# Optimization experiments

Hardware: AMD Instinct MI355X
Metric: run time of the kernel (lower is better)

The kernel has to match this reference:

```python
import jax, jax.numpy as jnp
import numpy as np

# Config (mirrors CorrLayerDownsample(J=3, L=8, A=1, A_prime=1, M=256, N=256,
# num_channels=1, shift_mode='samec', mask_angles=4)). With samec + 1 channel,
# every pair is 'shifted' (mask index 1) and groups (j1,j2) are contiguous in
# the global moment order, so concatenation reproduces results_storage order.
J, L, A, M, N, NB = 3, 8, 1, 256, 256, 2
MASK_ANGLES = 4
RADII = (1, 2)  # dyadic shift radii (assumed form of create_masks_shift)

def _mask_positions():
    # shift mask 1: origin plus shifts along mask_angles directions at dyadic radii
    pos = {(0, 0)}
    for k in range(MASK_ANGLES):
        th = np.pi * k / MASK_ANGLES
        for r in RADII:
            pos.add((int(round(r * np.cos(th))), int(round(r * np.sin(th)))))
    return sorted(pos)

def _union_flat_idx(h, w):
    # row-major flat indices of the union shift mask at resolution (h, w),
    # matching torch boolean-mask indexing order (mask_downsample + mask_idx_map_1)
    return np.array(sorted(((dx % h) * w + (dy % w)) for dx, dy in _mask_positions()), dtype=np.int64)

UNION_IDX = [_union_flat_idx(M >> j, N >> j) for j in range(J)]
NSHIFT = len(UNION_IDX[0])

# per-(j1,j2) channel gather indices: la = A*L*c + A*l + a = l (A=1, c=0)
# loop order in compute_idx: l1 outer, l2 inner
LA1 = np.repeat(np.arange(L), L)
LA2 = np.tile(np.arange(L), L)

def _spectral_pad(xh, Mn, Nn):
    # zero-pad Fourier representation to (Mn, Nn) -- spectral upsampling
    m, n = xh.shape[-2], xh.shape[-1]
    if (m, n) == (Mn, Nn):
        return xh
    xs = jnp.fft.fftshift(xh, axes=(-2, -1))
    ph, pw = (Mn - m) // 2, (Nn - n) // 2
    pad = [(0, 0)] * (xh.ndim - 2) + [(ph, ph), (pw, pw)]
    xp = jnp.pad(xs, pad)
    return jnp.fft.ifftshift(xp, axes=(-2, -1)) * ((Mn * Nn) / (m * n))

def _forward(xpsi_0, xpsi_1, xpsi_2):
    xs = [xpsi_0, xpsi_1, xpsi_2]
    hats = [jnp.fft.fft2(x.astype(jnp.complex64)) for x in xs]  # [nb, C, h_j, w_j]
    la1 = jnp.asarray(LA1)
    la2 = jnp.asarray(LA2)
    outs = []
    for j1 in range(J):
        h, w = M >> j1, N >> j1
        uidx = jnp.asarray(UNION_IDX[j1])
        h1 = hats[j1][:, la1]  # [nb, P=L*L, h, w]
        for j2 in range(j1, J):
            h2 = hats[j2][:, la2]
            if j2 > j1:
                h2 = _spectral_pad(h2, h, w)  # upsample coarser scale to scale j1
            corr = jnp.fft.ifft2(h1 * jnp.conj(h2)).real  # cross-correlation map
            flat = corr.reshape(corr.shape[0], corr.shape[1], h * w)
            outs.append(flat[:, :, uidx])  # masked downsample: keep shift positions
    return jnp.concatenate(outs, axis=1)  # [nb, total_pairs, NSHIFT]

def setup_inputs():
    key = jax.random.key(0)
    ks = jax.random.split(key, 3)
    return {
        "xpsi_0": jax.random.normal(ks[0], (NB, A * L, M, N), dtype=jnp.float32),
        "xpsi_1": jax.random.normal(ks[1], (NB, A * L, M // 2, N // 2), dtype=jnp.float32),
        "xpsi_2": jax.random.normal(ks[2], (NB, A * L, M // 4, N // 4), dtype=jnp.float32),
    }

def reference(xpsi_0, xpsi_1, xpsi_2):
    return _forward(xpsi_0, xpsi_1, xpsi_2)
```

## Files before the change

### kernel.cpp

```cpp
#include <hip/hip_runtime.h>

#define PI_D 3.14159265358979323846
#define PI_F 3.14159265358979323846f


__device__ inline float rtab_val(int n, int m2, int t) {
  if (t == 0) return 1.0f;
  double th = PI_D * (double)t / (double)n;
  double v = sin(th * (double)(m2 - 1)) / sin(th) + cos(th * (double)m2);
  return (float)(v / (double)m2);
}

__global__ __launch_bounds__(256) void k_front(
    const float* __restrict__ X0, const float* __restrict__ X1,
    const float* __restrict__ X2, float* __restrict__ P1p,
    float* __restrict__ P2p, float* __restrict__ V01, float* __restrict__ V02,
    float* __restrict__ V12, float* __restrict__ T01, float* __restrict__ T02,
    float* __restrict__ T12, float* __restrict__ out) {
  __shared__ float fsm[2304];
  int bid = blockIdx.x;
  int t = threadIdx.x;
  if (bid == 512) {
    for (int i = t; i < 5376; i += 256) out[i] = 0.f;
    return;
  }
  if (bid < 192) {
    const float* X; float* P; int lg, nsp, idx0;
    if (bid < 128) { X = X1; P = P1p; lg = 7; nsp = 8; idx0 = bid; }
    else           { X = X2; P = P2p; lg = 6; nsp = 4; idx0 = bid - 128; }
    int ch = idx0 / nsp, split = idx0 % nsp;
    int n = 1 << lg;
    int total = n * n;
    int chunk = total / nsp;
    int b0 = split * chunk;
    const float* x = X + (size_t)ch * total + b0;
    float s = 0.f;
    for (int i = t; i < chunk; i += 256) {
      int idx = b0 + i;
      float v = x[i];
      s += (((idx >> lg) ^ idx) & 1) ? -v : v;
    }
#pragma unroll
    for (int off = 32; off > 0; off >>= 1) s += __shfl_down(s, off, 64);
    __shared__ float red[4];
    if ((t & 63) == 0) red[t >> 6] = s;
    __syncthreads();
    if (t == 0) P[ch * nsp + split] = red[0] + red[1] + red[2] + red[3];
    return;
  }
  if (bid < 320) {
    int idx = bid - 192;
    int ch = idx >> 3, nxg = (idx & 7) * 16;
    float* Rl = fsm;
    float* Xs = fsm + 256;
    for (int i = t; i < 256; i += 256) Rl[i] = rtab_val(256, 128, i);
    const float4* xch4 =
        (const float4*)(X1 + (size_t)ch * 16384 + (size_t)nxg * 128);
    for (int i = t; i < 512; i += 256) ((float4*)Xs)[i] = xch4[i];
    __syncthreads();
    if (idx == 0)
      for (int i = t; i < 256; i += 256) T01[i] = Rl[i];
    float* vch = V01 + (size_t)ch * 128 * 256;
    for (int i = t; i < 2048; i += 256) {
      int r = i >> 7, k = i & 127;
      vch[(size_t)(nxg + r) * 256 + 2 * k] = Xs[r * 128 + k];
    }
    int cid = t & 63, wq = t >> 6;
    int m0 = 2 * cid + 1, m1 = 2 * cid + 129;
    float acc[4][2];
#pragma unroll
    for (int r = 0; r < 4; ++r) { acc[r][0] = 0.f; acc[r][1] = 0.f; }
    for (int ny = 0; ny < 128; ++ny) {
      float r0 = Rl[(m0 - 2 * ny) & 255];
      float r1 = Rl[(m1 - 2 * ny) & 255];
#pragma unroll
      for (int r = 0; r < 4; ++r) {
        float xv = Xs[(4 * wq + r) * 128 + ny];
        acc[r][0] += xv * r0;
        acc[r][1] += xv * r1;
      }
    }
#pragma unroll
    for (int r = 0; r < 4; ++r) {
      vch[(size_t)(nxg + 4 * wq + r) * 256 + m0] = acc[r][0];
      vch[(size_t)(nxg + 4 * wq + r) * 256 + m1] = acc[r][1];
    }
    return;
  }
  {
    int vbid = bid - 320;
    const float* X = X2; float* V;
    int n1, n2, s, ch, nxg, colh;
    if (vbid < 128) {
      V = V02; n1 = 256; n2 = 64; s = 4;
      ch = vbid >> 3; nxg = ((vbid >> 1) & 3) * 16; colh = vbid & 1;
    } else {
      int w = vbid - 128;
      V = V12; n1 = 128; n2 = 64; s = 2;
      ch = w >> 2; nxg = (w & 3) * 16; colh = 0;
    }
    float* Rl = fsm;
    float* Xs = fsm + 256;
    for (int i = t; i < n1; i += 256) Rl[i] = rtab_val(n1, n2, i);
    const float4* xch4 =
        (const float4*)(X + (size_t)ch * n2 * n2 + (size_t)nxg * n2);
    int nx4 = (16 * n2) >> 2;
    for (int i = t; i < nx4; i += 256) ((float4*)Xs)[i] = xch4[i];
    __syncthreads();
    if (vbid == 0)
      for (int i = t; i < 256; i += 256) T02[i] = Rl[i];
    if (vbid == 128)
      for (int i = t; i < 128; i += 256) T12[i] = Rl[i];
    int myq = (t & 63) + colh * 128;
    int nxq = t >> 6;
    int mask = n1 - 1;
    float acc[4][2];
#pragma unroll
    for (int r = 0; r < 4; ++r)
#pragma unroll
      for (int c = 0; c < 2; ++c) acc[r][c] = 0.f;
    for (int ny = 0; ny < n2; ++ny) {
      float xv[4];
#pragma unroll
      for (int r = 0; r < 4; ++r) xv[r] = Xs[(4 * nxq + r) * n2 + ny];
#pragma unroll
      for (int c = 0; c < 2; ++c) {
        float rv = Rl[(myq + 64 * c - s * ny) & mask];
#pragma unroll
        for (int r = 0; r < 4; ++r) acc[r][c] += xv[r] * rv;
      }
    }
    float* vch = V + (size_t)ch * n2 * n1;
#pragma unroll
    for (int r = 0; r < 4; ++r)
      for (int c = 0; c < 2; ++c)
        vch[(size_t)(nxg + 4 * nxq + r) * n1 + myq + 64 * c] = acc[r][c];
  }
}

__global__ __launch_bounds__(256) void k_main(const float* __restrict__ X0,
                                              const float* __restrict__ X1,
                                              const float* __restrict__ X2,
                                              const float* __restrict__ V01,
                                              const float* __restrict__ V02,
                                              const float* __restrict__ V12,
                                              const float* __restrict__ P1p,
                                              const float* __restrict__ P2p,
                                              const float* __restrict__ T01,
                                              const float* __restrict__ T02,
                                              const float* __restrict__ T12,
                                              float* __restrict__ out) {
  __shared__ float sRl[256];
  __shared__ float sh[4864];
  __shared__ float Vs[2][2048];
  int u = blockIdx.x;
  int t = threadIdx.x;
  int lane = t & 63;
  int wv = t >> 6;

  float accC[8][7];
#pragma unroll
  for (int i = 0; i < 8; ++i)
#pragma unroll
    for (int p = 0; p < 7; ++p) accC[i][p] = 0.f;

  int b, l2, base;

  if (u < 640) {
    const float* V; const float* Pp; const float* A1b; const float* T;
    int n1, n2, s, ch, chunk, nsp, lgn1; float inv;
    if (u < 256) {
      V = V01; Pp = P1p; nsp = 8; A1b = X0; n1 = 256; n2 = 128; s = 2;
      inv = 1.f / 16384.f; ch = u >> 4; chunk = u & 15; lgn1 = 8; base = 64;
      T = T01;
    } else if (u < 512) {
      int w = u - 256;
      V = V02; Pp = P2p; nsp = 4; A1b = X0; n1 = 256; n2 = 64; s = 4;
      inv = 1.f / 4096.f; ch = w >> 4; chunk = w & 15; lgn1 = 8; base = 128;
      T = T02;
    } else {
      int w = u - 512;
      V = V12; Pp = P2p; nsp = 4; A1b = X1; n1 = 128; n2 = 64; s = 2;
      inv = 1.f / 4096.f; ch = w >> 3; chunk = w & 7; lgn1 = 7; base = 256;
      T = T12;
    }
    int mask = n1 - 1;
    for (int i = t; i < n1; i += 256) sRl[i] = T[i];
    int mxg = chunk * 16;
    b = ch >> 3; l2 = ch & 7;
    const float* vch = V + (size_t)ch * n2 * n1;
    float Pv = 0.f;
    for (int i = 0; i < nsp; ++i) Pv += Pp[ch * nsp + i];
    float a = PI_F / (float)s;
    int per = 2 * s;

    if (n1 == 256) {
      if (s == 2) {
        for (int i = t; i < 640; i += 256) {
          int rl = 2 * (i >> 6), c4 = (i & 63) * 4;
          int mx = (mxg - 2 + rl) & 255;
          *(float4*)&sh[rl * 256 + c4] =
              *(const float4*)(vch + (size_t)(mx >> 1) * 256 + c4);
        }
      } else {
        for (int i = t; i < 320; i += 256) {
          int rl = 2 + 4 * (i >> 6), c4 = (i & 63) * 4;
          int mx = (mxg - 2 + rl) & 255;
          *(float4*)&sh[rl * 256 + c4] =
              *(const float4*)(vch + (size_t)(mx >> 2) * 256 + c4);
        }
      }
    } else {
      for (int i = t; i < 320; i += 256) {
        int rl = 2 * (i >> 5), c4 = (i & 31) * 4;
        int mx = (mxg - 2 + rl) & 127;
        *(float4*)&sh[rl * 128 + c4] =
            *(const float4*)(vch + (size_t)(mx >> 1) * 128 + c4);
      }
    }

    int nr, rls[4];
    if (s == 2) {
      if (wv == 0)      { nr = 3; rls[0] = 1;  rls[1] = 3;  rls[2] = 5;  rls[3] = 1; }
      else if (wv == 1) { nr = 2; rls[0] = 7;  rls[1] = 9;  rls[2] = 7;  rls[3] = 7; }
      else if (wv == 2) { nr = 2; rls[0] = 11; rls[1] = 13; rls[2] = 11; rls[3] = 11; }
      else              { nr = 2; rls[0] = 15; rls[1] = 17; rls[2] = 15; rls[3] = 15; }
    } else {
      if (wv == 0)      { nr = 4; rls[0] = 0;  rls[1] = 1;  rls[2] = 3;  rls[3] = 4; }
      else if (wv == 1) { nr = 4; rls[0] = 5;  rls[1] = 7;  rls[2] = 8;  rls[3] = 9; }
      else if (wv == 2) { nr = 3; rls[0] = 11; rls[1] = 12; rls[2] = 13; rls[3] = 11; }
      else              { nr = 3; rls[0] = 15; rls[1] = 16; rls[2] = 17; rls[3] = 15; }
    }
    int bj[4];
#pragma unroll
    for (int j = 0; j < 4; ++j) bj[j] = (mxg - 2 + rls[j]) & mask;

    const float4* vp4 = (const float4*)vch;
    if (n1 == 256) {
      int ntl = n2 >> 3;
      for (int i = t; i < 512; i += 256) ((float4*)Vs[0])[i] = vp4[i];
      __syncthreads();
      float4 acc[4];
#pragma unroll
      for (int j = 0; j < 4; ++j) acc[j] = make_float4(0.f, 0.f, 0.f, 0.f);
      for (int tl = 0; tl < ntl; ++tl) {
        float4 stg0, stg1;
        bool has = (tl + 1 < ntl);
        if (has) {
          stg0 = vp4[(size_t)(tl + 1) * 512 + t];
          stg1 = vp4[(size_t)(tl + 1) * 512 + 256 + t];
        }
        const float* Vc = Vs[tl & 1];
        int tb = tl * 8;
#pragma unroll
        for (int kk = 0; kk < 8; ++kk) {
          float4 vv = *(const float4*)&Vc[kk * 256 + 4 * lane];
          int ss = s * (tb + kk);
#pragma unroll
          for (int j = 0; j < 4; ++j)
            if (j < nr) {
              float rv = sRl[(bj[j] - ss) & 255];
              acc[j].x += rv * vv.x;
              acc[j].y += rv * vv.y;
              acc[j].z += rv * vv.z;
              acc[j].w += rv * vv.w;
            }
        }
        if (has) {
          float4* d = (float4*)Vs[(tl & 1) ^ 1];
          d[t] = stg0;
          d[256 + t] = stg1;
        }
        __syncthreads();
      }
      float smy[4];
#pragma unroll
      for (int j = 0; j < 4; ++j)
        smy[j] = sinf(a * (float)((4 * lane + j) & (per - 1)));
#pragma unroll
      for (int j = 0; j < 4; ++j)
        if (j < nr) {
          float q = inv * sinf(a * (float)(bj[j] & (per - 1))) * Pv;
          float4 o = acc[j];
          o.x -= q * smy[0];
          o.y -= q * smy[1];
          o.z -= q * smy[2];
          o.w -= q * smy[3];
          *(float4*)&sh[rls[j] * 256 + 4 * lane] = o;
        }
    } else {
      for (int i = t; i < 256; i += 256) ((float4*)Vs[0])[i] = vp4[i];
      __syncthreads();
      float2 acc[4];
#pragma unroll
      for (int j = 0; j < 4; ++j) acc[j] = make_float2(0.f, 0.f);
      for (int tl = 0; tl < 8; ++tl) {
        float4 stg0;
        bool has = (tl + 1 < 8);
        if (has) stg0 = vp4[(size_t)(tl + 1) * 256 + t];
        const float* Vc = Vs[tl & 1];
        int tb = tl * 8;
#pragma unroll
        for (int kk = 0; kk < 8; ++kk) {
          float2 vv = *(const float2*)&Vc[kk * 128 + 2 * lane];
          int ss = 2 * (tb + kk);
#pragma unroll
          for (int j = 0; j < 4; ++j)
            if (j < nr) {
              float rv = sRl[(bj[j] - ss) & 127];
              acc[j].x += rv * vv.x;
              acc[j].y += rv * vv.y;
            }
        }
        if (has) ((float4*)Vs[(tl & 1) ^ 1])[t] = stg0;
        __syncthreads();
      }
      const float a2 = PI_F * 0.5f;
      float smy0 = sinf(a2 * (float)((2 * lane) & 3));
      float smy1 = sinf(a2 * (float)((2 * lane + 1) & 3));
#pragma unroll
      for (int j = 0; j < 4; ++j)
        if (j < nr) {
          float q = inv * sinf(a2 * (float)(bj[j] & 3)) * Pv;
          float2 o = acc[j];
          o.x -= q * smy0;
          o.y -= q * smy1;
          *(float2*)&sh[rls[j] * 128 + 2 * lane] = o;
        }
    }
    __syncthreads();

    int lgtpr = lgn1 - 2;
    int tpr = 1 << lgtpr;
    int rif = 256 >> lgtpr;
    int rid = t >> lgtpr;
    int cid2 = t & (tpr - 1);
    int ty = cid2 * 4;
    int tym = (ty - 4) & mask;
    int n1sq = n1 * n1;
    const float* A1 = A1b + (size_t)(b * 8) * n1sq;
    for (int rr = 0; rr < 16; rr += rif) {
      int ri = rr + rid;
      const float* r0 = &sh[(ri + 2) * n1];
      const float* r1 = &sh[(ri + 1) * n1];
      const float* r2 = &sh[ri * n1];
      const float* r3 = &sh[(ri + 3) * n1];
      float4 a0 = *(const float4*)(r0 + tym);
      float4 b0 = *(const float4*)(r0 + ty);
      float4 a1 = *(const float4*)(r1 + tym);
      float4 b1 = *(const float4*)(r1 + ty);
      float4 b2 = *(const float4*)(r2 + ty);
      float4 a3 = *(const float4*)(r3 + tym);
      float4 b3 = *(const float4*)(r3 + ty);
      const float* rA = A1 + (size_t)(mxg + ri) * n1 + ty;
#pragma unroll
      for (int l1 = 0; l1 < 8; ++l1) {
        float4 xv = *(const float4*)(rA + (size_t)l1 * n1sq);
        accC[l1][0] += xv.x * b0.x + xv.y * b0.y + xv.z * b0.z + xv.w * b0.w;
        accC[l1][1] += xv.x * a0.w + xv.y * b0.x + xv.z * b0.y + xv.w * b0.z;
        accC[l1][2] += xv.x * a0.z + xv.y * a0.w + xv.z * b0.x + xv.w * b0.y;
        accC[l1][3] += xv.x * b1.x + xv.y * b1.y + xv.z * b1.z + xv.w * b1.w;
        accC[l1][4] += xv.x * a1.w + xv.y * b1.x + xv.z * b1.y + xv.w * b1.z;
        accC[l1][5] += xv.x * b2.x + xv.y * b2.y + xv.z * b2.z + xv.w * b2.w;
        accC[l1][6] += xv.x * a3.w + xv.y * b3.x + xv.z * b3.y + xv.w * b3.z;
      }
    }
  } else {
    int w = u - 640;
    const float* Ab; int loc, lgn1, lgc;
    if (w < 256)      { loc = w;       Ab = X0; lgn1 = 8; lgc = 4; base = 0;   }
    else if (w < 384) { loc = w - 256; Ab = X1; lgn1 = 7; lgc = 3; base = 192; }
    else              { loc = w - 384; Ab = X2; lgn1 = 6; lgc = 2; base = 320; }
    int n1 = 1 << lgn1;
    int mask = n1 - 1;
    int n1sq = n1 * n1;
    int chunk = loc & ((1 << lgc) - 1);
    int bl2 = loc >> lgc;
    b = bl2 >> 3; l2 = bl2 & 7;
    const float* A1 = Ab + (size_t)(b * 8) * n1sq;
    const float* A2 = Ab + (size_t)(b * 8 + l2) * n1sq;
    int lgtpr = lgn1 - 2;
    int tpr = 1 << lgtpr;
    int rif = 256 >> lgtpr;
    int rid = t >> lgtpr;
    int cid2 = t & (tpr - 1);
    int ty = cid2 * 4;
    int tym = (ty - 4) & mask;
    for (int rr = 0; rr < 16; rr += rif) {
      int row = chunk * 16 + rr + rid;
      const float* r0 = A2 + (size_t)row * n1;
      const float* r1 = A2 + (size_t)((row - 1) & mask) * n1;
      const float* r2 = A2 + (size_t)((row - 2) & mask) * n1;
      const float* r3 = A2 + (size_t)((row + 1) & mask) * n1;
      float4 a0 = *(const float4*)(r0 + tym);
      float4 b0 = *(const float4*)(r0 + ty);
      float4 a1 = *(const float4*)(r1 + tym);
      float4 b1 = *(const float4*)(r1 + ty);
      float4 b2 = *(const float4*)(r2 + ty);
      float4 a3 = *(const float4*)(r3 + tym);
      float4 b3 = *(const float4*)(r3 + ty);
      const float* rA = A1 + (size_t)row * n1 + ty;
#pragma unroll
      for (int l1 = 0; l1 < 8; ++l1) {
        float4 xv = *(const float4*)(rA + (size_t)l1 * n1sq);
        accC[l1][0] += xv.x * b0.x + xv.y * b0.y + xv.z * b0.z + xv.w * b0.w;
        accC[l1][1] += xv.x * a0.w + xv.y * b0.x + xv.z * b0.y + xv.w * b0.z;
        accC[l1][2] += xv.x * a0.z + xv.y * a0.w + xv.z * b0.x + xv.w * b0.y;
        accC[l1][3] += xv.x * b1.x + xv.y * b1.y + xv.z * b1.z + xv.w * b1.w;
        accC[l1][4] += xv.x * a1.w + xv.y * b1.x + xv.z * b1.y + xv.w * b1.z;
        accC[l1][5] += xv.x * b2.x + xv.y * b2.y + xv.z * b2.z + xv.w * b2.w;
        accC[l1][6] += xv.x * a3.w + xv.y * b3.x + xv.z * b3.y + xv.w * b3.z;
      }
    }
  }

  float* af = &accC[0][0];
#pragma unroll
  for (int j = 0; j < 56; ++j) {
    float v = af[j];
    v += __shfl_down(v, 32, 64);
    v += __shfl_down(v, 16, 64);
    af[j] = v;
  }
  __syncthreads();
  if (lane < 16) {
    float* rowp = sh + (wv * 16 + lane) * 60;
#pragma unroll
    for (int j = 0; j < 14; ++j)
      *(float4*)&rowp[4 * j] =
          make_float4(af[4 * j], af[4 * j + 1], af[4 * j + 2], af[4 * j + 3]);
  }
  __syncthreads();
  if (t < 224) {
    int v = t >> 2, q = t & 3;
    float s2 = 0.f;
#pragma unroll
    for (int i = 0; i < 16; ++i) s2 += sh[(q * 16 + i) * 60 + v];
    s2 += __shfl_down(s2, 2, 64);
    s2 += __shfl_down(s2, 1, 64);
    if (q == 0) {
      int l1o = v / 7, p = v % 7;
      atomicAdd(&out[((size_t)b * 384 + base + l1o * 8 + l2) * 7 + p], s2);
    }
  }
}

extern "C" void kernel_launch(void* const* d_in, const int* in_sizes, int n_in,
                              void* d_out, int out_size, void* d_ws, size_t ws_size,
                              hipStream_t stream) {
  const float* X0 = (const float*)d_in[0];
  const float* X1 = (const float*)d_in[1];
  const float* X2 = (const float*)d_in[2];
  float* out = (float*)d_out;
  float* ws = (float*)d_ws;

  float* V01 = ws + 2359296;
  float* V02 = ws + 2883584;
  float* V12 = ws + 3145728;
  float* P1p = ws + 3276800;
  float* P2p = ws + 3276928;
  float* T01 = ws + 3276992;
  float* T02 = ws + 3277248;
  float* T12 = ws + 3277504;

  k_front<<<513, 256, 0, stream>>>(X0, X1, X2, P1p, P2p, V01, V02, V12, T01,
                                   T02, T12, out);
  k_main<<<1088, 256, 0, stream>>>(X0, X1, X2, V01, V02, V12, P1p, P2p, T01,
                                   T02, T12, out);
}
```

Measured before the change: 107.2 us.

## Stage same-scale rows in shared memory and unify correlation path; halve V staging buffer

Same-scale blocks now stage the 19 needed rows of the shifted operand into shared memory, then run the same shared-memory correlation loop as the cross-scale blocks. This replaces the repeated uncached global reads of neighbouring rows with one coalesced load per block. The double-buffered V tile shrinks to 1024 floats per buffer, with twice as many smaller pipeline steps, to cut LDS use and possibly raise occupancy. The cost is more barriers in the cross-scale loop and a staging step plus barrier in the same-scale blocks.

```diff
diff --git a/kernel.cpp b/kernel.cpp
--- a/kernel.cpp
+++ b/kernel.cpp
@@ -152,23 +152,18 @@
                                               float* __restrict__ out) {
   __shared__ float sRl[256];
   __shared__ float sh[4864];
-  __shared__ float Vs[2][2048];
+  __shared__ float Vs[2][1024];
   int u = blockIdx.x;
   int t = threadIdx.x;
   int lane = t & 63;
   int wv = t >> 6;
 
-  float accC[8][7];
-#pragma unroll
-  for (int i = 0; i < 8; ++i)
-#pragma unroll
-    for (int p = 0; p < 7; ++p) accC[i][p] = 0.f;
-
-  int b, l2, base;
+  int b, l2, base, lgn1, mxg;
+  const float* A1b;
 
   if (u < 640) {
-    const float* V; const float* Pp; const float* A1b; const float* T;
-    int n1, n2, s, ch, chunk, nsp, lgn1; float inv;
+    const float* V; const float* Pp; const float* T;
+    int n1, n2, s, ch, chunk, nsp; float inv;
     if (u < 256) {
       V = V01; Pp = P1p; nsp = 8; A1b = X0; n1 = 256; n2 = 128; s = 2;
       inv = 1.f / 16384.f; ch = u >> 4; chunk = u & 15; lgn1 = 8; base = 64;
@@ -186,7 +181,7 @@
     }
     int mask = n1 - 1;
     for (int i = t; i < n1; i += 256) sRl[i] = T[i];
-    int mxg = chunk * 16;
+    mxg = chunk * 16;
     b = ch >> 3; l2 = ch & 7;
     const float* vch = V + (size_t)ch * n2 * n1;
     float Pv = 0.f;
@@ -237,25 +232,21 @@
 
     const float4* vp4 = (const float4*)vch;
     if (n1 == 256) {
-      int ntl = n2 >> 3;
-      for (int i = t; i < 512; i += 256) ((float4*)Vs[0])[i] = vp4[i];
+      int ntl = n2 >> 2;
+      ((float4*)Vs[0])[t] = vp4[t];
       __syncthreads();
       float4 acc[4];
 #pragma unroll
       for (int j = 0; j < 4; ++j) acc[j] = make_float4(0.f, 0.f, 0.f, 0.f);
       for (int tl = 0; tl < ntl; ++tl) {
-        float4 stg0, stg1;
+        float4 stg;
         bool has = (tl + 1 < ntl);
-        if (has) {
-          stg0 = vp4[(size_t)(tl + 1) * 512 + t];
-          stg1 = vp4[(size_t)(tl + 1) * 512 + 256 + t];
-        }
+        if (has) stg = vp4[(size_t)(tl + 1) * 256 + t];
         const float* Vc = Vs[tl & 1];
-        int tb = tl * 8;
-#pragma unroll
-        for (int kk = 0; kk < 8; ++kk) {
+#pragma unroll
+        for (int kk = 0; kk < 4; ++kk) {
           float4 vv = *(const float4*)&Vc[kk * 256 + 4 * lane];
-          int ss = s * (tb + kk);
+          int ss = s * (4 * tl + kk);
 #pragma unroll
           for (int j = 0; j < 4; ++j)
             if (j < nr) {
@@ -266,11 +257,7 @@
               acc[j].w += rv * vv.w;
             }
         }
-        if (has) {
-          float4* d = (float4*)Vs[(tl & 1) ^ 1];
-          d[t] = stg0;
-          d[256 + t] = stg1;
-        }
+        if (has) ((float4*)Vs[(tl & 1) ^ 1])[t] = stg;
         __syncthreads();
       }
       float smy[4];
@@ -289,21 +276,20 @@
           *(float4*)&sh[rls[j] * 256 + 4 * lane] = o;
         }
     } else {
-      for (int i = t; i < 256; i += 256) ((float4*)Vs[0])[i] = vp4[i];
+      if (t < 128) ((float4*)Vs[0])[t] = vp4[t];
       __syncthreads();
       float2 acc[4];
 #pragma unroll
       for (int j = 0; j < 4; ++j) acc[j] = make_float2(0.f, 0.f);
-      for (int tl = 0; tl < 8; ++tl) {
-        float4 stg0;
-        bool has = (tl + 1 < 8);
-        if (has) stg0 = vp4[(size_t)(tl + 1) * 256 + t];
+      for (int tl = 0; tl < 16; ++tl) {
+        float4 stg;
+        bool has = (tl + 1 < 16) && (t < 128);
+        if (has) stg = vp4[(size_t)(tl + 1) * 128 + t];
         const float* Vc = Vs[tl & 1];
-        int tb = tl * 8;
-#pragma unroll
-        for (int kk = 0; kk < 8; ++kk) {
+#pragma unroll
+        for (int kk = 0; kk < 4; ++kk) {
           float2 vv = *(const float2*)&Vc[kk * 128 + 2 * lane];
-          int ss = 2 * (tb + kk);
+          int ss = 2 * (4 * tl + kk);
 #pragma unroll
           for (int j = 0; j < 4; ++j)
             if (j < nr) {
@@ -312,7 +298,7 @@
               acc[j].y += rv * vv.y;
             }
         }
-        if (has) ((float4*)Vs[(tl & 1) ^ 1])[t] = stg0;
+        if (has) ((float4*)Vs[(tl & 1) ^ 1])[t] = stg;
         __syncthreads();
       }
       const float a2 = PI_F * 0.5f;
@@ -328,8 +314,41 @@
           *(float2*)&sh[rls[j] * 128 + 2 * lane] = o;
         }
     }
-    __syncthreads();
-
+  } else {
+    int w = u - 640;
+    const float* Ab; int loc, lgc;
+    if (w < 256)      { loc = w;       Ab = X0; lgn1 = 8; lgc = 4; base = 0;   }
+    else if (w < 384) { loc = w - 256; Ab = X1; lgn1 = 7; lgc = 3; base = 192; }
+    else              { loc = w - 384; Ab = X2; lgn1 = 6; lgc = 2; base = 320; }
+    int n1 = 1 << lgn1;
+    int mask = n1 - 1;
+    int n1sq = n1 * n1;
+    int chunk = loc & ((1 << lgc) - 1);
+    int bl2 = loc >> lgc;
+    b = bl2 >> 3; l2 = bl2 & 7;
+    A1b = Ab;
+    const float* A2 = Ab + (size_t)(b * 8 + l2) * n1sq;
+    mxg = chunk * 16;
+    int nst = (19 * n1) >> 2;
+    int l2n1 = lgn1 - 2;
+    for (int i = t; i < nst; i += 256) {
+      int rl = i >> l2n1;
+      int c4 = (i & ((n1 >> 2) - 1)) * 4;
+      int src = (mxg - 2 + rl) & mask;
+      *(float4*)&sh[rl * n1 + c4] = *(const float4*)(A2 + (size_t)src * n1 + c4);
+    }
+  }
+  __syncthreads();
+
+  float accC[8][7];
+#pragma unroll
+  for (int i = 0; i < 8; ++i)
+#pragma unroll
+    for (int p = 0; p < 7; ++p) accC[i][p] = 0.f;
+  {
+    int n1 = 1 << lgn1;
+    int mask = n1 - 1;
+    int n1sq = n1 * n1;
     int lgtpr = lgn1 - 2;
     int tpr = 1 << lgtpr;
     int rif = 256 >> lgtpr;
@@ -337,7 +356,6 @@
     int cid2 = t & (tpr - 1);
     int ty = cid2 * 4;
     int tym = (ty - 4) & mask;
-    int n1sq = n1 * n1;
     const float* A1 = A1b + (size_t)(b * 8) * n1sq;
     for (int rr = 0; rr < 16; rr += rif) {
       int ri = rr + rid;
@@ -365,53 +383,6 @@
         accC[l1][6] += xv.x * a3.w + xv.y * b3.x + xv.z * b3.y + xv.w * b3.z;
       }
     }
-  } else {
-    int w = u - 640;
-    const float* Ab; int loc, lgn1, lgc;
-    if (w < 256)      { loc = w;       Ab = X0; lgn1 = 8; lgc = 4; base = 0;   }
-    else if (w < 384) { loc = w - 256; Ab = X1; lgn1 = 7; lgc = 3; base = 192; }
-    else              { loc = w - 384; Ab = X2; lgn1 = 6; lgc = 2; base = 320; }
-    int n1 = 1 << lgn1;
-    int mask = n1 - 1;
-    int n1sq = n1 * n1;
-    int chunk = loc & ((1 << lgc) - 1);
-    int bl2 = loc >> lgc;
-    b = bl2 >> 3; l2 = bl2 & 7;
-    const float* A1 = Ab + (size_t)(b * 8) * n1sq;
-    const float* A2 = Ab + (size_t)(b * 8 + l2) * n1sq;
-    int lgtpr = lgn1 - 2;
-    int tpr = 1 << lgtpr;
-    int rif = 256 >> lgtpr;
-    int rid = t >> lgtpr;
-    int cid2 = t & (tpr - 1);
-    int ty = cid2 * 4;
-    int tym = (ty - 4) & mask;
-    for (int rr = 0; rr < 16; rr += rif) {
-      int row = chunk * 16 + rr + rid;
-      const float* r0 = A2 + (size_t)row * n1;
-      const float* r1 = A2 + (size_t)((row - 1) & mask) * n1;
-      const float* r2 = A2 + (size_t)((row - 2) & mask) * n1;
-      const float* r3 = A2 + (size_t)((row + 1) & mask) * n1;
-      float4 a0 = *(const float4*)(r0 + tym);
-      float4 b0 = *(const float4*)(r0 + ty);
-      float4 a1 = *(const float4*)(r1 + tym);
-      float4 b1 = *(const float4*)(r1 + ty);
-      float4 b2 = *(const float4*)(r2 + ty);
-      float4 a3 = *(const float4*)(r3 + tym);
-      float4 b3 = *(const float4*)(r3 + ty);
-      const float* rA = A1 + (size_t)row * n1 + ty;
-#pragma unroll
-      for (int l1 = 0; l1 < 8; ++l1) {
-        float4 xv = *(const float4*)(rA + (size_t)l1 * n1sq);
-        accC[l1][0] += xv.x * b0.x + xv.y * b0.y + xv.z * b0.z + xv.w * b0.w;
-        accC[l1][1] += xv.x * a0.w + xv.y * b0.x + xv.z * b0.y + xv.w * b0.z;
-        accC[l1][2] += xv.x * a0.z + xv.y * a0.w + xv.z * b0.x + xv.w * b0.y;
-        accC[l1][3] += xv.x * b1.x + xv.y * b1.y + xv.z * b1.z + xv.w * b1.w;
-        accC[l1][4] += xv.x * a1.w + xv.y * b1.x + xv.z * b1.y + xv.w * b1.z;
-        accC[l1][5] += xv.x * b2.x + xv.y * b2.y + xv.z * b2.z + xv.w * b2.w;
-        accC[l1][6] += xv.x * a3.w + xv.y * b3.x + xv.z * b3.y + xv.w * b3.z;
-      }
-    }
   }
 
   float* af = &accC[0][0];
```

Result: faster. 94.93 us (-11.5%).
